# Kernel tuning notes

Measured on AMD Instinct MI355X. Metric: run time of the kernel, lower is better.

The kernel has to match this reference:

```python
import jax, jax.numpy as jnp
import numpy as np

B, S, IN, H, OUT = 2048, 512, 1, 64, 72


def setup_inputs() -> dict:
    key = jax.random.key(0)
    ks = jax.random.split(key, 11)
    s = 1.0 / np.sqrt(H)  # pytorch default init scale
    return {
        "x": jax.random.normal(ks[0], (B, S, IN), dtype=jnp.float32),
        "W_ih_l0": jax.random.normal(ks[1], (4 * H, IN), dtype=jnp.float32) * s,
        "W_hh_l0": jax.random.normal(ks[2], (4 * H, H), dtype=jnp.float32) * s,
        "b_ih_l0": jax.random.normal(ks[3], (4 * H,), dtype=jnp.float32) * s,
        "b_hh_l0": jax.random.normal(ks[4], (4 * H,), dtype=jnp.float32) * s,
        "W_ih_l1": jax.random.normal(ks[5], (4 * H, H), dtype=jnp.float32) * s,
        "W_hh_l1": jax.random.normal(ks[6], (4 * H, H), dtype=jnp.float32) * s,
        "b_ih_l1": jax.random.normal(ks[7], (4 * H,), dtype=jnp.float32) * s,
        "b_hh_l1": jax.random.normal(ks[8], (4 * H,), dtype=jnp.float32) * s,
        "fc_w": jax.random.normal(ks[9], (OUT, H), dtype=jnp.float32) * s,
        "fc_b": jax.random.normal(ks[10], (OUT,), dtype=jnp.float32) * s,
    }


def _lstm_layer(x_sbF, W_ih, W_hh, b_ih, b_hh):
    # x_sbF: [S, B, F]; returns all hidden states [S, B, H].
    Hh = W_hh.shape[1]
    Bb = x_sbF.shape[1]
    # precompute input projections for all timesteps (one big GEMM)
    xg = jnp.einsum('sbf,gf->sbg', x_sbF, W_ih) + (b_ih + b_hh)  # [S, B, 4H]

    def step(carry, xg_t):
        h, c = carry
        gates = xg_t + h @ W_hh.T  # [B, 4H], pytorch gate order i,f,g,o
        i, f, g, o = jnp.split(gates, 4, axis=-1)
        i = jax.nn.sigmoid(i)
        f = jax.nn.sigmoid(f)
        g = jnp.tanh(g)
        o = jax.nn.sigmoid(o)
        c = f * c + i * g
        h = o * jnp.tanh(c)
        return (h, c), h

    h0 = jnp.zeros((Bb, Hh), dtype=x_sbF.dtype)
    c0 = jnp.zeros((Bb, Hh), dtype=x_sbF.dtype)
    _, hs = jax.lax.scan(step, (h0, c0), xg)
    return hs  # [S, B, H]


def reference(x, W_ih_l0, W_hh_l0, b_ih_l0, b_hh_l0,
              W_ih_l1, W_hh_l1, b_ih_l1, b_hh_l1, fc_w, fc_b):
    # x: [B, S, 1] (batch_first). Dropout(0.2) between layers is identity in eval mode.
    xs = jnp.transpose(x, (1, 0, 2))  # [S, B, IN]
    h1 = _lstm_layer(xs, W_ih_l0, W_hh_l0, b_ih_l0, b_hh_l0)  # [S, B, H]
    h2 = _lstm_layer(h1, W_ih_l1, W_hh_l1, b_ih_l1, b_hh_l1)  # [S, B, H]
    last = h2[-1]  # [B, H] == out[:, -1, :]
    return last @ fc_w.T + fc_b  # [B, OUT]
```

## Files before the change

kernel.cpp:

```cpp
#include <hip/hip_runtime.h>


#define BATCH 2048
#define SEQ   512
#define HIDN  64
#define NOUT  72
#define BT    4
#define NT    512
#define L2E   1.4426950408889634f

typedef _Float16 f16x8 __attribute__((ext_vector_type(8)));
typedef float    f32x4 __attribute__((ext_vector_type(4)));

__device__ __forceinline__ float fast_rcp(float x){ return __builtin_amdgcn_rcpf(x); }
__device__ __forceinline__ float exp2_hw(float x){ float r; asm("v_exp_f32 %0, %1" : "=v"(r) : "v"(x)); return r; }
__device__ __forceinline__ float exp2_neg_hw(float x){ float r; asm("v_exp_f32 %0, -%1" : "=v"(r) : "v"(x)); return r; }
__device__ __forceinline__ float sigm2(float s){ return fast_rcp(1.f + exp2_neg_hw(s)); }
__device__ __forceinline__ float tanh2(float s){ return fmaf(-2.f, fast_rcp(exp2_hw(s) + 1.f), 1.f); }

__device__ __forceinline__ float swap_pick(float a, float b){
    unsigned ua = __float_as_uint(a), ub = __float_as_uint(b);
    asm volatile("v_permlane32_swap_b32 %0, %1" : "+v"(ua), "+v"(ub));
    return __uint_as_float(ua);
}

__global__ __launch_bounds__(NT, 4)
void lstm2_mfma_kernel(const float* __restrict__ x,
                       const float* __restrict__ wih0,
                       const float* __restrict__ whh0,
                       const float* __restrict__ bih0,
                       const float* __restrict__ bhh0,
                       const float* __restrict__ wih1,
                       const float* __restrict__ whh1,
                       const float* __restrict__ bih1,
                       const float* __restrict__ bhh1,
                       const float* __restrict__ fcw,
                       const float* __restrict__ fcb,
                       float* __restrict__ out)
{
    const int t    = threadIdx.x;
    const int lane = t & 63;
    const int w    = t >> 6;
    const int wq   = w & 3;
    const int lyr  = w >> 2;
    const int l15  = lane & 15;
    const int lg   = lane >> 4;
    const int b0   = blockIdx.x * BT;
    const int hidb = wq * 16;

    __shared__ float x_sb[SEQ][BT];
    __shared__ __align__(16) _Float16 fragA[2][4][32][8];
    __shared__ float h_fc[BT][HIDN + 1];

    f16x8 bw[4][4];
    float bsum[4], wx[4];
    #pragma unroll
    for (int q = 0; q < 4; ++q) {
        const float sc = (q == 2) ? (2.f * L2E) : L2E;
        const int c = q*64 + hidb + l15;
        if (lyr == 0) {
            #pragma unroll
            for (int kc = 0; kc < 2; ++kc) {
                const float* src = whh0 + c*HIDN + kc*32 + lg*8;
                f16x8 v;
                #pragma unroll
                for (int e = 0; e < 8; ++e) v[e] = (_Float16)(src[e] * sc);
                bw[q][kc] = v;
            }
            bsum[q] = (bih0[c] + bhh0[c]) * sc;
            wx[q]   = wih0[c] * sc;
        } else {
            #pragma unroll
            for (int kc = 0; kc < 4; ++kc) {
                const float* src = (kc < 2) ? (wih1 + c*HIDN + kc*32 + lg*8)
                                            : (whh1 + c*HIDN + (kc-2)*32 + lg*8);
                f16x8 v;
                #pragma unroll
                for (int e = 0; e < 8; ++e) v[e] = (_Float16)(src[e] * sc);
                bw[q][kc] = v;
            }
            bsum[q] = (bih1[c] + bhh1[c]) * sc;
            wx[q]   = 0.f;
        }
    }

    for (int i = t; i < BT * SEQ; i += NT) {
        int b = i >> 9, s = i & (SEQ - 1);
        x_sb[s][b] = x[(size_t)(b0 + b) * SEQ + s];
    }
    {
        unsigned* fz = (unsigned*)fragA;
        for (int i = t; i < 1024; i += NT) fz[i] = 0u;
    }
    __syncthreads();

    const int srow = lane >> 4;
    const int hh   = hidb + l15;
    const int kcs  = lyr * 2 + (hh >> 5);
    const int eW   = hh & 7;
    const int g5   = (hh >> 3) & 3;
    const int slot_rd = lg * 8 + (lane & 7);
    float cst = 0.f;

    #pragma unroll 1
    for (int k = 0; k <= SEQ; ++k) {
        const int buf = k & 1, nbuf = buf ^ 1;

        f32x4 acc[4];
        #pragma unroll
        for (int q = 0; q < 4; ++q) acc[q] = f32x4{bsum[q], bsum[q], bsum[q], bsum[q]};

        if (lyr == 0) {
            f16x8 a0 = *(const f16x8*)&fragA[buf][0][slot_rd][0];
            f16x8 a1 = *(const f16x8*)&fragA[buf][1][slot_rd][0];
            #pragma unroll
            for (int q = 0; q < 4; ++q) {
                acc[q] = __builtin_amdgcn_mfma_f32_16x16x32_f16(a0, bw[q][0], acc[q], 0, 0, 0);
                acc[q] = __builtin_amdgcn_mfma_f32_16x16x32_f16(a1, bw[q][1], acc[q], 0, 0, 0);
            }
        } else {
            f16x8 a[4];
            #pragma unroll
            for (int kc = 0; kc < 4; ++kc)
                a[kc] = *(const f16x8*)&fragA[buf][kc][slot_rd][0];
            #pragma unroll
            for (int kc = 0; kc < 4; ++kc) {
                #pragma unroll
                for (int q = 0; q < 4; ++q)
                    acc[q] = __builtin_amdgcn_mfma_f32_16x16x32_f16(a[kc], bw[q][kc], acc[q], 0, 0, 0);
            }
        }

        const bool do_state = lyr ? (k > 0) : (k < SEQ);
        if (do_state) {
            float g4[4];
            #pragma unroll
            for (int q = 0; q < 4; ++q) {
                float t0  = swap_pick(acc[q][0], acc[q][2]);
                float t1  = swap_pick(acc[q][1], acc[q][3]);
                float t1s = __shfl_xor(t1, 16);
                g4[q] = (lane & 16) ? t1s : t0;
            }
            float pi = g4[0], pf = g4[1], pg = g4[2], po = g4[3];
            if (lyr == 0) {
                float xv = x_sb[k][srow];
                pi = fmaf(wx[0], xv, pi); pf = fmaf(wx[1], xv, pf);
                pg = fmaf(wx[2], xv, pg); po = fmaf(wx[3], xv, po);
            }
            float iv = sigm2(pi), fv = sigm2(pf), gv = tanh2(pg), ov = sigm2(po);
            cst = fmaf(fv, cst, iv * gv);
            float h = ov * tanh2(cst * (2.f * L2E));
            fragA[nbuf][kcs][g5*8 + srow][eW] = (_Float16)h;
            if (lyr == 1 && k == SEQ) h_fc[srow][hh] = h;
        }
        __syncthreads();
    }

    for (int idx = t; idx < BT * NOUT; idx += NT) {
        int b = idx / NOUT, o = idx - b * NOUT;
        float a = fcb[o];
        #pragma unroll
        for (int j = 0; j < HIDN; ++j) a = fmaf(h_fc[b][j], fcw[o * HIDN + j], a);
        out[(size_t)(b0 + b) * NOUT + o] = a;
    }
}

extern "C" void kernel_launch(void* const* d_in, const int* in_sizes, int n_in,
                              void* d_out, int out_size, void* d_ws, size_t ws_size,
                              hipStream_t stream) {
    const float* x    = (const float*)d_in[0];
    const float* wih0 = (const float*)d_in[1];
    const float* whh0 = (const float*)d_in[2];
    const float* bih0 = (const float*)d_in[3];
    const float* bhh0 = (const float*)d_in[4];
    const float* wih1 = (const float*)d_in[5];
    const float* whh1 = (const float*)d_in[6];
    const float* bih1 = (const float*)d_in[7];
    const float* bhh1 = (const float*)d_in[8];
    const float* fcw  = (const float*)d_in[9];
    const float* fcb  = (const float*)d_in[10];
    float* out = (float*)d_out;

    dim3 grid(BATCH / BT);
    dim3 block(NT);
    hipLaunchKernelGGL(lstm2_mfma_kernel, grid, block, 0, stream,
                       x, wih0, whh0, bih0, bhh0, wih1, whh1, bih1, bhh1,
                       fcw, fcb, out);
}
```

Measured before the change: 489.7 us.

## Process eight batch rows per block with duplicated wave sets per half

Doubles the batch rows per block to 8 and the threads to 1024. Two groups of eight waves each redundantly run the same MFMAs and each group extracts a different half of the accumulator rows. This removes the cross-lane shuffle and select from the gate extraction and fills more of the MFMA's 16 rows with real batch entries, halving the grid. In exchange every MFMA is computed twice, and the per-step barrier now spans 16 waves.

```diff
diff --git a/kernel.cpp b/kernel.cpp
--- a/kernel.cpp
+++ b/kernel.cpp
@@ -5,8 +5,8 @@
 #define SEQ   512
 #define HIDN  64
 #define NOUT  72
-#define BT    4
-#define NT    512
+#define BT    8
+#define NT    1024
 #define L2E   1.4426950408889634f
 
 typedef _Float16 f16x8 __attribute__((ext_vector_type(8)));
@@ -41,8 +41,10 @@
     const int t    = threadIdx.x;
     const int lane = t & 63;
     const int w    = t >> 6;
-    const int wq   = w & 3;
-    const int lyr  = w >> 2;
+    const int v    = w & 7;
+    const int half = w >> 3;
+    const int wq   = v & 3;
+    const int lyr  = v >> 2;
     const int l15  = lane & 15;
     const int lg   = lane >> 4;
     const int b0   = blockIdx.x * BT;
@@ -57,27 +59,27 @@
     #pragma unroll
     for (int q = 0; q < 4; ++q) {
         const float sc = (q == 2) ? (2.f * L2E) : L2E;
-        const int c = q*64 + hidb + l15;
+        const int c = q * 64 + hidb + l15;
         if (lyr == 0) {
             #pragma unroll
             for (int kc = 0; kc < 2; ++kc) {
-                const float* src = whh0 + c*HIDN + kc*32 + lg*8;
-                f16x8 v;
+                const float* src = whh0 + c * HIDN + kc * 32 + lg * 8;
+                f16x8 vv;
                 #pragma unroll
-                for (int e = 0; e < 8; ++e) v[e] = (_Float16)(src[e] * sc);
-                bw[q][kc] = v;
+                for (int e = 0; e < 8; ++e) vv[e] = (_Float16)(src[e] * sc);
+                bw[q][kc] = vv;
             }
             bsum[q] = (bih0[c] + bhh0[c]) * sc;
             wx[q]   = wih0[c] * sc;
         } else {
             #pragma unroll
             for (int kc = 0; kc < 4; ++kc) {
-                const float* src = (kc < 2) ? (wih1 + c*HIDN + kc*32 + lg*8)
-                                            : (whh1 + c*HIDN + (kc-2)*32 + lg*8);
-                f16x8 v;
+                const float* src = (kc < 2) ? (wih1 + c * HIDN + kc * 32 + lg * 8)
+                                            : (whh1 + c * HIDN + (kc - 2) * 32 + lg * 8);
+                f16x8 vv;
                 #pragma unroll
-                for (int e = 0; e < 8; ++e) v[e] = (_Float16)(src[e] * sc);
-                bw[q][kc] = v;
+                for (int e = 0; e < 8; ++e) vv[e] = (_Float16)(src[e] * sc);
+                bw[q][kc] = vv;
             }
             bsum[q] = (bih1[c] + bhh1[c]) * sc;
             wx[q]   = 0.f;
@@ -90,11 +92,12 @@
     }
     {
         unsigned* fz = (unsigned*)fragA;
-        for (int i = t; i < 1024; i += NT) fz[i] = 0u;
+        if (t < 1024) fz[t] = 0u;
     }
     __syncthreads();
 
-    const int srow = lane >> 4;
+    const int bb   = ((lane >> 4) & 1) * 4 + (lane >> 5) * 2;
+    const int row  = bb + half;
     const int hh   = hidb + l15;
     const int kcs  = lyr * 2 + (hh >> 5);
     const int eW   = hh & 7;
@@ -134,24 +137,24 @@
         const bool do_state = lyr ? (k > 0) : (k < SEQ);
         if (do_state) {
             float g4[4];
-            #pragma unroll
-            for (int q = 0; q < 4; ++q) {
-                float t0  = swap_pick(acc[q][0], acc[q][2]);
-                float t1  = swap_pick(acc[q][1], acc[q][3]);
-                float t1s = __shfl_xor(t1, 16);
-                g4[q] = (lane & 16) ? t1s : t0;
+            if (half == 0) {
+                #pragma unroll
+                for (int q = 0; q < 4; ++q) g4[q] = swap_pick(acc[q][0], acc[q][2]);
+            } else {
+                #pragma unroll
+                for (int q = 0; q < 4; ++q) g4[q] = swap_pick(acc[q][1], acc[q][3]);
             }
             float pi = g4[0], pf = g4[1], pg = g4[2], po = g4[3];
             if (lyr == 0) {
-                float xv = x_sb[k][srow];
+                float xv = x_sb[k][row];
                 pi = fmaf(wx[0], xv, pi); pf = fmaf(wx[1], xv, pf);
                 pg = fmaf(wx[2], xv, pg); po = fmaf(wx[3], xv, po);
             }
             float iv = sigm2(pi), fv = sigm2(pf), gv = tanh2(pg), ov = sigm2(po);
             cst = fmaf(fv, cst, iv * gv);
             float h = ov * tanh2(cst * (2.f * L2E));
-            fragA[nbuf][kcs][g5*8 + srow][eW] = (_Float16)h;
-            if (lyr == 1 && k == SEQ) h_fc[srow][hh] = h;
+            fragA[nbuf][kcs][g5 * 8 + row][eW] = (_Float16)h;
+            if (lyr == 1 && k == SEQ) h_fc[row][hh] = h;
         }
         __syncthreads();
     }
```

New measurement: 440.2 us. -10.1%, faster.
